# Optimization experiments

Measured on AMD Instinct MI355X. Metric: run time of the kernel, lower is better.

## Reference

```python
import jax, jax.numpy as jnp
import numpy as np

D = 64      # node_input_dim == node_hidden_dim
EIN = 16    # edge_input_dim
EH = 64     # edge_hidden_dim
NL, NR = 5000, 15000
EL, ER = 50000, 150000
STEPS = 6
EPS = 1e-5
SLOPE = 0.01


def _ln(x, g, b):
    mu = jnp.mean(x, axis=-1, keepdims=True)
    v = jnp.mean((x - mu) ** 2, axis=-1, keepdims=True)
    return (x - mu) / jnp.sqrt(v + EPS) * g + b


def _lrelu(x):
    return jnp.where(x > 0, x, SLOPE * x)


def setup_inputs() -> dict:
    key = jax.random.key(0)
    ks = jax.random.split(key, 32)

    def n(k, shape, fan_in):
        return jax.random.normal(k, shape, jnp.float32) * (fan_in ** -0.5)

    return {
        'lig_n_feat': jax.random.normal(ks[0], (NL, D), jnp.float32),
        'lig_e_feat': jax.random.normal(ks[1], (EL, EIN), jnp.float32),
        'lig_src': jax.random.randint(ks[2], (EL,), 0, NL),
        'lig_dst': jax.random.randint(ks[3], (EL,), 0, NL),
        'rec_n_feat': jax.random.normal(ks[4], (NR, D), jnp.float32),
        'rec_e_feat': jax.random.normal(ks[5], (ER, EIN), jnp.float32),
        'rec_src': jax.random.randint(ks[6], (ER,), 0, NR),
        'rec_dst': jax.random.randint(ks[7], (ER,), 0, NR),
        'mask': jax.random.uniform(ks[8], (NL, NR), jnp.float32),
        # linear0
        'W0': n(ks[9], (D, D), D), 'b0': jnp.zeros((D,), jnp.float32),
        # edge network: Linear(EIN,EH) -> ReLU -> Linear(EH, D*D)
        'We1': n(ks[10], (EH, EIN), EIN), 'be1': jnp.zeros((EH,), jnp.float32),
        'We2': n(ks[11], (D * D, EH), EH), 'be2': jnp.zeros((D * D,), jnp.float32),
        # NNConv residual fc (no bias) and conv bias
        'resW': n(ks[12], (D, D), D), 'conv_b': jnp.zeros((D,), jnp.float32),
        # message layer Linear(2D, D)
        'msgW': n(ks[13], (D, 2 * D), 2 * D), 'msgb': jnp.zeros((D,), jnp.float32),
        # attention projections (no bias)
        'Qlig': n(ks[14], (D, D), D), 'Klig': n(ks[15], (D, D), D), 'Vlig': n(ks[16], (D, D), D),
        'Qrec': n(ks[17], (D, D), D), 'Krec': n(ks[18], (D, D), D), 'Vrec': n(ks[19], (D, D), D),
        # final LayerNorms
        'g_lig': jnp.ones((D,), jnp.float32), 'b_lig': jnp.zeros((D,), jnp.float32),
        'g_rec': jnp.ones((D,), jnp.float32), 'b_rec': jnp.zeros((D,), jnp.float32),
    }


def _gather_branch(x, efeat, src, dst, n_nodes, W0, b0, We1, be1, We2, be2, resW, conv_b, msgW, msgb):
    # per-edge weight matrices from edge MLP: [E, D, D] (in x out)
    We = jax.nn.relu(efeat @ We1.T + be1) @ We2.T + be2
    We = We.reshape(-1, D, D)
    h = jax.nn.relu(x @ W0.T + b0)
    for _ in range(STEPS):
        msg = jnp.einsum('ei,eio->eo', h[src], We)          # gather + per-edge transform
        agg = jax.ops.segment_sum(msg, dst, num_segments=n_nodes)  # scatter-sum
        m = jax.nn.relu(agg + h @ resW.T + conv_b)           # NNConv residual + bias, relu
        h = jnp.concatenate([m, h], axis=1) @ msgW.T + msgb  # message_layer
    return h + x


def reference(lig_n_feat, lig_e_feat, lig_src, lig_dst, rec_n_feat, rec_e_feat, rec_src, rec_dst,
              mask, W0, b0, We1, be1, We2, be2, resW, conv_b, msgW, msgb,
              Qlig, Klig, Vlig, Qrec, Krec, Vrec, g_lig, b_lig, g_rec, b_rec):
    lig_Fv = _gather_branch(lig_n_feat, lig_e_feat, lig_src, lig_dst, NL,
                            W0, b0, We1, be1, We2, be2, resW, conv_b, msgW, msgb)
    rec_Fv = _gather_branch(rec_n_feat, rec_e_feat, rec_src, rec_dst, NR,
                            W0, b0, We1, be1, We2, be2, resW, conv_b, msgW, msgb)
    hl = _ln(lig_Fv, g_lig, b_lig)
    hr = _ln(rec_Fv, g_rec, b_rec)
    # lig attends to rec
    ql, kr, vr = _lrelu(hl @ Qlig.T), _lrelu(hr @ Krec.T), hr @ Vrec.T
    a = mask * (ql @ kr.T) - 1000.0 * (1.0 - mask)
    att_lig = jax.nn.softmax(a, axis=1) @ vr
    # rec attends to lig
    qr, kl, vl = _lrelu(hr @ Qrec.T), _lrelu(hl @ Klig.T), hl @ Vlig.T
    mt = mask.T
    a2 = mt * (qr @ kl.T) - 1000.0 * (1.0 - mt)
    att_rec = jax.nn.softmax(a2, axis=1) @ vl
    return (_ln(att_lig, g_lig, b_lig), _ln(att_rec, g_rec, b_rec))
```

## Files before the change

### kernel.cpp

```cpp
#include <hip/hip_runtime.h>
#include <hip/hip_bf16.h>

typedef unsigned short ushort_t;
typedef __attribute__((ext_vector_type(8))) short short8_t;
typedef __attribute__((ext_vector_type(4))) float f32x4;
typedef __attribute__((ext_vector_type(4))) unsigned uint4_t;

#define NLIG 5000
#define NREC 15000
#define NTOT 20000
#define ELIG 50000
#define EREC 150000
#define ETOT 200000
#define VSTRIDE 20160

__device__ __forceinline__ float us2f(ushort_t u){
  union { float f; unsigned int i; } x; x.i = ((unsigned int)u) << 16; return x.f;
}
__device__ __forceinline__ ushort_t f2us(float f){
  __hip_bfloat16 b = __float2bfloat16(f);
  return *reinterpret_cast<ushort_t*>(&b);
}
__device__ __forceinline__ unsigned pkbf(float a, float b){
  return (unsigned)f2us(a) | ((unsigned)f2us(b) << 16);
}
__device__ __forceinline__ float wsum64(float v){
#pragma unroll
  for (int s = 32; s >= 1; s >>= 1) v += __shfl_xor(v, s, 64);
  return v;
}
__device__ __forceinline__ f32x4 mfma32(short8_t a, short8_t b, f32x4 c){
  return __builtin_amdgcn_mfma_f32_16x16x32_bf16(a, b, c, 0, 0, 0);
}
__device__ __forceinline__ int geti(const int* __restrict__ p, int i, int i64){
  return i64 ? p[2*i] : p[i];
}

__global__ void kdetect2(const unsigned* __restrict__ xw, const unsigned* __restrict__ iw,
                         int* __restrict__ flagp){
  const int lane = threadIdx.x;
  unsigned w = xw[lane];
  int e0 = (int)((w >> 7) & 0xFF);
  int hit = (e0 >= 100 && e0 <= 134) ? 1 : 0;
  int zodd = ((lane & 1) && iw[lane] == 0u) ? 1 : 0;
#pragma unroll
  for (int s = 32; s >= 1; s >>= 1){
    hit  += __shfl_xor(hit,  s, 64);
    zodd += __shfl_xor(zodd, s, 64);
  }
  if (lane == 0){
    flagp[0] = (hit  >= 40) ? 1 : 0;
    flagp[1] = (zodd >= 24) ? 1 : 0;
  }
}

__global__ void ksent(float* __restrict__ out, int n, float c){
  int i = blockIdx.x*256 + threadIdx.x;
  if (i < n) out[i] = c;
}

__global__ void kcvt_x(const void* __restrict__ lx, const void* __restrict__ rx,
                       const int* __restrict__ flagp, float* __restrict__ xall){
  const int flag = flagp[0];
  const int idx = blockIdx.x*256 + threadIdx.x;
  const void* src; int local;
  if (idx < NLIG*64){ src = lx; local = idx; } else { src = rx; local = idx - NLIG*64; }
  float v;
  if (flag) v = us2f(((const ushort_t*)src)[local]);
  else      v = ((const float*)src)[local];
  xall[idx] = v;
}

struct Srcs { const void* p[20]; };
__global__ void kcvt_w(Srcs S, const int* __restrict__ flagp, float* __restrict__ wcvt){
  const int bounds[21] = {0,4096,4160,5184,5248,267392,271488,275584,275648,283840,
                          283904,288000,292096,296192,300288,304384,308480,308544,308608,308672,308736};
  const int flag = flagp[0];
  const int idx = blockIdx.x*256 + threadIdx.x;
  if (idx >= 308736) return;
  int seg = 0;
#pragma unroll
  for (int s = 1; s < 20; ++s) if (idx >= bounds[s]) seg = s;
  const void* src = S.p[0];
#pragma unroll
  for (int s = 1; s < 20; ++s) if (seg == s) src = S.p[s];
  const int local = idx - bounds[seg];
  float v;
  if (flag) v = us2f(((const ushort_t*)src)[local]);
  else      v = ((const float*)src)[local];
  wcvt[idx] = v;
}

#define W_W0    0
#define W_B0    4096
#define W_WE1   4160
#define W_BE1   5184
#define W_WE2   5248
#define W_BE2   267392
#define W_RESW  271488
#define W_CONVB 275584
#define W_MSGW  275648
#define W_MSGB  283840
#define W_QLIG  283904
#define W_KLIG  288000
#define W_VLIG  292096
#define W_QREC  296192
#define W_KREC  300288
#define W_VREC  304384
#define W_GLIG  308480
#define W_BLIG  308544
#define W_GREC  308608
#define W_BREC  308672

__global__ void kWpk(const float* __restrict__ We2f, ushort_t* __restrict__ Wpk){
  int oidx = blockIdx.x*256 + threadIdx.x;
  int j = oidx & 7, lane = (oidx >> 3) & 63, p = (oidx >> 9) & 1;
  int t = (oidx >> 10) & 3, kb = oidx >> 12;
  int o = t*16 + (lane & 15);
  int gik = kb*32 + (lane >> 4)*8 + j;
  int i = gik >> 6, k = gik & 63;
  float v = We2f[(size_t)(i*64 + o)*64 + k];
  ushort_t hi = f2us(v);
  Wpk[oidx] = p ? f2us(v - us2f(hi)) : hi;
}

__global__ void kh0(const float* __restrict__ xall, const float* __restrict__ W0f,
                    const float* __restrict__ b0f, float* __restrict__ h){
  __shared__ float xr[4][64];
  const int lane = threadIdx.x & 63, wv = threadIdx.x >> 6;
  const int n = blockIdx.x*4 + wv;
  xr[wv][lane] = xall[(size_t)n*64 + lane];
  __syncthreads();
  float acc = b0f[lane];
  const float* wr = W0f + lane*64;
#pragma unroll
  for (int i = 0; i < 64; ++i) acc += xr[wv][i] * wr[i];
  h[(size_t)n*64 + lane] = acc > 0.f ? acc : 0.f;
}

__global__ void khist(const int* __restrict__ ldst, const int* __restrict__ rdst,
                      const int* __restrict__ flagp, int* __restrict__ counts){
  const int i64 = flagp[1];
  const int e = blockIdx.x*256 + threadIdx.x;
  if (e >= ETOT) return;
  int dstg = (e < ELIG) ? geti(ldst, e, i64) : geti(rdst, e - ELIG, i64) + NLIG;
  atomicAdd(&counts[dstg], 1);
}

__global__ __launch_bounds__(1024) void kscan(const int* __restrict__ counts, int* __restrict__ offs){
  __shared__ int part[1024];
  const int tid = threadIdx.x;
  const int PER = 20;
  int loc[PER]; int s = 0;
#pragma unroll
  for (int j = 0; j < PER; ++j){ int idx = tid*PER + j; int v = (idx < NTOT) ? counts[idx] : 0; loc[j] = s; s += v; }
  part[tid] = s;
  __syncthreads();
  for (int d = 1; d < 1024; d <<= 1){
    int add = (tid >= d) ? part[tid - d] : 0;
    __syncthreads();
    part[tid] += add;
    __syncthreads();
  }
  int pre = (tid > 0) ? part[tid - 1] : 0;
#pragma unroll
  for (int j = 0; j < PER; ++j){ int idx = tid*PER + j; if (idx < NTOT) offs[idx] = pre + loc[j]; }
  if (tid == 1023) offs[NTOT] = part[1023];
}

__global__ void kfill(const int* __restrict__ lsrc, const int* __restrict__ ldst,
                      const int* __restrict__ rsrc, const int* __restrict__ rdst,
                      const void* __restrict__ lef, const void* __restrict__ ref_,
                      const int* __restrict__ offs, int* __restrict__ cursor,
                      const int* __restrict__ flagp,
                      int* __restrict__ e_srcn, float* __restrict__ ef_srt){
  const int flag = flagp[0];
  const int i64  = flagp[1];
  const int e = blockIdx.x*256 + threadIdx.x;
  if (e >= ETOT) return;
  int srcg, dstg, le; const void* efb;
  if (e < ELIG){ srcg = geti(lsrc, e, i64); dstg = geti(ldst, e, i64); efb = lef; le = e; }
  else {
    int e2 = e - ELIG;
    srcg = geti(rsrc, e2, i64) + NLIG; dstg = geti(rdst, e2, i64) + NLIG; efb = ref_; le = e2;
  }
  int pos = offs[dstg] + atomicAdd(&cursor[dstg], 1);
  e_srcn[pos] = srcg;
  float* efd = ef_srt + (size_t)pos*16;
  if (flag){
    const ushort_t* efp = (const ushort_t*)efb + (size_t)le*16;
#pragma unroll
    for (int c = 0; c < 16; ++c) efd[c] = us2f(efp[c]);
  } else {
    const float* efp = (const float*)efb + (size_t)le*16;
#pragma unroll
    for (int c = 0; c < 16; ++c) efd[c] = efp[c];
  }
}

__global__ __launch_bounds__(1024)
void kstep(const float* __restrict__ hin, float* __restrict__ hout,
           const int* __restrict__ offs, const int* __restrict__ e_srcn,
           const float* __restrict__ ef_srt,
           const ushort_t* __restrict__ Wpk,
           const float* __restrict__ We1f, const float* __restrict__ be1f,
           const float* __restrict__ resWf, const float* __restrict__ convbf,
           const float* __restrict__ msgWf, const float* __restrict__ msgbf,
           const float* __restrict__ be2f){
  __shared__ alignas(16) char sbuf[65536];
  __shared__ float h_lds[1024];
  __shared__ float Hs_lds[1024];
  __shared__ float m_lds[1024];
  __shared__ float cbf[64], mbf[64];

  const int tid = threadIdx.x, lane = tid & 63, wv = tid >> 6;
  const int n0 = blockIdx.x * 16;

  h_lds[tid] = hin[(size_t)n0*64 + tid];
  if (tid < 64){ cbf[tid] = convbf[tid]; mbf[tid] = msgbf[tid]; }

  float w1r[16];
#pragma unroll
  for (int c = 0; c < 16; ++c) w1r[c] = We1f[lane*16 + c];
  const float b1 = be1f[lane];

  float sacc[64];
#pragma unroll
  for (int i = 0; i < 64; ++i) sacc[i] = 0.f;
  float hs = 0.f;
  {
    const int v = n0 + wv;
    const int jb = offs[v], je = offs[v+1];
    for (int j = jb; j < je; ++j){
      const int sn = e_srcn[j];
      const float* efp = ef_srt + (size_t)j*16;
      float zl = b1;
#pragma unroll
      for (int c = 0; c < 16; ++c) zl += efp[c] * w1r[c];
      zl = zl > 0.f ? zl : 0.f;
      hs += hin[(size_t)sn*64 + lane];
      const float4* hp = (const float4*)(hin + (size_t)sn*64);
#pragma unroll
      for (int i4 = 0; i4 < 16; ++i4){
        float4 hv = hp[i4];
        sacc[i4*4+0] += hv.x * zl;
        sacc[i4*4+1] += hv.y * zl;
        sacc[i4*4+2] += hv.z * zl;
        sacc[i4*4+3] += hv.w * zl;
      }
    }
    Hs_lds[wv*64 + lane] = hs;
  }

  const int r15 = lane & 15, g4 = lane >> 4;
  const int tW = wv & 3, kq = wv >> 2;
  f32x4 acc; acc[0]=0.f; acc[1]=0.f; acc[2]=0.f; acc[3]=0.f;
  const unsigned sswz = ((unsigned)(wv & 7)) << 4;
  const unsigned rswz = ((unsigned)(r15 & 7)) << 4;
#pragma unroll
  for (int c = 0; c < 4; ++c){
#pragma unroll
    for (int ii = 0; ii < 16; ++ii){
      float v = sacc[c*16 + ii];
      ushort_t hi16 = f2us(v);
      unsigned off = ((unsigned)(wv*2048 + (ii*64 + lane)*2)) ^ sswz;
      *(ushort_t*)(sbuf + off) = hi16;
      *(ushort_t*)(sbuf + 32768 + off) = f2us(v - us2f(hi16));
    }
    __syncthreads();
    for (int kk = 0; kk < 8; ++kk){
      const int lk = kq*256 + kk*32;
      const int kb = c*32 + kq*8 + kk;
      const unsigned aoff = ((unsigned)(r15*2048 + (lk + g4*8)*2)) ^ rswz;
      const short8_t ah = *(const short8_t*)(sbuf + aoff);
      const short8_t al = *(const short8_t*)(sbuf + 32768 + aoff);
      const ushort_t* bp = Wpk + (size_t)(kb*4 + tW)*1024 + lane*8;
      const short8_t bh = *(const short8_t*)(bp);
      const short8_t bl = *(const short8_t*)(bp + 512);
      acc = mfma32(ah, bh, acc);
      acc = mfma32(ah, bl, acc);
      acc = mfma32(al, bh, acc);
    }
    __syncthreads();
  }

  float* redf  = (float*)sbuf;
  float* be2s  = (float*)(sbuf + 16384);
  float* resWt = (float*)(sbuf + 32768);
#pragma unroll
  for (int q = 0; q < 4; ++q)
    redf[kq*1024 + (g4*4 + q)*64 + tW*16 + r15] = acc[q];
  for (int idx = tid; idx < 4096; idx += 1024){
    be2s[idx] = be2f[idx];
    resWt[(idx & 63)*65 + (idx >> 6)] = resWf[idx];
  }
  __syncthreads();
  {
    float aggv = cbf[lane];
#pragma unroll
    for (int k4 = 0; k4 < 4; ++k4) aggv += redf[k4*1024 + wv*64 + lane];
    float t1 = 0.f, t2 = 0.f;
#pragma unroll 8
    for (int i = 0; i < 64; ++i){
      t1 += Hs_lds[wv*64 + i] * be2s[i*64 + lane];
      t2 += h_lds[wv*64 + i]  * resWt[i*65 + lane];
    }
    float mv = aggv + t1 + t2;
    m_lds[wv*64 + lane] = mv > 0.f ? mv : 0.f;
  }
  __syncthreads();
  float* msgWt = (float*)sbuf;
  for (int idx = tid; idx < 8192; idx += 1024)
    msgWt[(idx & 127)*65 + (idx >> 7)] = msgWf[idx];
  __syncthreads();
  {
    float hn = mbf[lane];
#pragma unroll 8
    for (int i = 0; i < 64; ++i){
      hn += m_lds[wv*64 + i] * msgWt[i*65 + lane];
      hn += h_lds[wv*64 + i] * msgWt[(64 + i)*65 + lane];
    }
    hout[(size_t)(n0 + wv)*64 + lane] = hn;
  }
}

__global__ void kfvproj(const float* __restrict__ h, const float* __restrict__ xall,
    const float* __restrict__ wcvt,
    ushort_t* __restrict__ qbh, ushort_t* __restrict__ qbl,
    ushort_t* __restrict__ kbh, ushort_t* __restrict__ kbl,
    ushort_t* __restrict__ vbT){
  __shared__ float hr[4][64];
  const int lane = threadIdx.x & 63, wv = threadIdx.x >> 6;
  const int n = blockIdx.x*4 + wv;
  const bool isLig = n < NLIG;
  const float fv = h[(size_t)n*64 + lane] + xall[(size_t)n*64 + lane];
  const float mu = wsum64(fv) * (1.f/64.f);
  const float dd = fv - mu;
  const float var = wsum64(dd*dd) * (1.f/64.f);
  const float gg = wcvt[(isLig ? W_GLIG : W_GREC) + lane];
  const float bb = wcvt[(isLig ? W_BLIG : W_BREC) + lane];
  const float hl = dd * rsqrtf(var + 1e-5f) * gg + bb;
  hr[wv][lane] = hl;
  __syncthreads();
  const float* Qw = wcvt + (isLig ? W_QLIG : W_QREC) + lane*64;
  const float* Kw = wcvt + (isLig ? W_KLIG : W_KREC) + lane*64;
  const float* Vw = wcvt + (isLig ? W_VLIG : W_VREC) + lane*64;
  float qa = 0.f, ka = 0.f, va = 0.f;
#pragma unroll
  for (int i = 0; i < 64; ++i){
    const float hv = hr[wv][i];
    qa += hv * Qw[i];
    ka += hv * Kw[i];
    va += hv * Vw[i];
  }
  qa = qa > 0.f ? qa : 0.01f*qa;
  ka = ka > 0.f ? ka : 0.01f*ka;
  const size_t o = (size_t)n*64 + lane;
  ushort_t qh = f2us(qa); qbh[o] = qh; qbl[o] = f2us(qa - us2f(qh));
  ushort_t kh = f2us(ka); kbh[o] = kh; kbl[o] = f2us(ka - us2f(kh));
  vbT[(size_t)lane*VSTRIDE + n] = f2us(va);
}

template<int DIRN>
__global__ __launch_bounds__(512, 2)
void kattn(const ushort_t* __restrict__ qbh, const ushort_t* __restrict__ qbl,
           const ushort_t* __restrict__ kbh, const ushort_t* __restrict__ kbl,
           const ushort_t* __restrict__ vbT, const void* __restrict__ maskp,
           const int* __restrict__ flagp,
           const float* __restrict__ gwf, const float* __restrict__ bwf,
           float* __restrict__ out){
  constexpr int R   = DIRN ? NREC : NLIG;
  constexpr int C   = DIRN ? NLIG : NREC;
  constexpr int RNB = DIRN ? NLIG : 0;
  constexpr int CNB = DIRN ? 0 : NLIG;
  __shared__ float mred[8][16], lred[8][16];
  __shared__ float ored[8][64][17];

  const int flag = flagp[0];
  const int tid = threadIdx.x, lane = tid & 63, wv = tid >> 6;
  const int r15 = lane & 15, g4 = lane >> 4;
  const int rbase = blockIdx.x * 16;
  int rn = rbase + r15; if (rn > R-1) rn = R-1;

  const ushort_t* qph = qbh + (size_t)(RNB + rn)*64;
  const ushort_t* qpl = qbl + (size_t)(RNB + rn)*64;
  const short8_t qh0a = *(const short8_t*)(qph + g4*8);
  const short8_t qh0b = *(const short8_t*)(qph + 32 + g4*8);
  const short8_t ql0a = *(const short8_t*)(qpl + g4*8);
  const short8_t ql0b = *(const short8_t*)(qpl + 32 + g4*8);

  const int srcA = (((g4 & 1) * 2)     << 4) + r15;
  const int srcB = (((g4 & 1) * 2 + 1) << 4) + r15;
  const bool hiBank = (g4 >> 1) != 0;

  float mrun = -1e30f, lrun = 0.f;
  f32x4 oacc[4];
#pragma unroll
  for (int t = 0; t < 4; ++t){ oacc[t][0]=0.f; oacc[t][1]=0.f; oacc[t][2]=0.f; oacc[t][3]=0.f; }

  for (int cb = wv*32; cb < C; cb += 256){
    int cn0 = cb + r15;      if (cn0 > C-1) cn0 = C-1;
    int cn1 = cb + 16 + r15; if (cn1 > C-1) cn1 = C-1;
    const ushort_t* kp0h = kbh + (size_t)(CNB + cn0)*64;
    const ushort_t* kp0l = kbl + (size_t)(CNB + cn0)*64;
    const ushort_t* kp1h = kbh + (size_t)(CNB + cn1)*64;
    const ushort_t* kp1l = kbl + (size_t)(CNB + cn1)*64;
    f32x4 st0; st0[0]=0.f; st0[1]=0.f; st0[2]=0.f; st0[3]=0.f;
    f32x4 st1 = st0;
    {
      short8_t ka_ = *(const short8_t*)(kp0h + g4*8);
      short8_t kb_ = *(const short8_t*)(kp0h + 32 + g4*8);
      st0 = mfma32(ka_, qh0a, st0); st0 = mfma32(kb_, qh0b, st0);
      st0 = mfma32(ka_, ql0a, st0); st0 = mfma32(kb_, ql0b, st0);
      short8_t kc_ = *(const short8_t*)(kp0l + g4*8);
      short8_t kd_ = *(const short8_t*)(kp0l + 32 + g4*8);
      st0 = mfma32(kc_, qh0a, st0); st0 = mfma32(kd_, qh0b, st0);
    }
    {
      short8_t ka_ = *(const short8_t*)(kp1h + g4*8);
      short8_t kb_ = *(const short8_t*)(kp1h + 32 + g4*8);
      st1 = mfma32(ka_, qh0a, st1); st1 = mfma32(kb_, qh0b, st1);
      st1 = mfma32(ka_, ql0a, st1); st1 = mfma32(kb_, ql0b, st1);
      short8_t kc_ = *(const short8_t*)(kp1l + g4*8);
      short8_t kd_ = *(const short8_t*)(kp1l + 32 + g4*8);
      st1 = mfma32(kc_, qh0a, st1); st1 = mfma32(kd_, qh0b, st1);
    }
    float sv0[4], sv1[4]; float tmax = -1e30f;
#pragma unroll
    for (int j = 0; j < 4; ++j){
      const int c0 = cb + g4*4 + j, c1 = cb + 16 + g4*4 + j;
      const int c0c = c0 > C-1 ? C-1 : c0, c1c = c1 > C-1 ? C-1 : c1;
      size_t m0, m1;
      if (DIRN == 0){ m0 = (size_t)rn*NREC + c0c; m1 = (size_t)rn*NREC + c1c; }
      else          { m0 = (size_t)c0c*NREC + rn; m1 = (size_t)c1c*NREC + rn; }
      float mv0, mv1;
      if (flag){ mv0 = us2f(((const ushort_t*)maskp)[m0]); mv1 = us2f(((const ushort_t*)maskp)[m1]); }
      else     { mv0 = ((const float*)maskp)[m0];          mv1 = ((const float*)maskp)[m1]; }
      sv0[j] = (c0 < C) ? mv0 * (st0[j] + 1000.f) : -1e30f;
      sv1[j] = (c1 < C) ? mv1 * (st1[j] + 1000.f) : -1e30f;
      tmax = fmaxf(tmax, fmaxf(sv0[j], sv1[j]));
    }
    tmax = fmaxf(tmax, __shfl_xor(tmax, 16, 64));
    tmax = fmaxf(tmax, __shfl_xor(tmax, 32, 64));
    const float mnew = fmaxf(mrun, tmax);
    const float corr = __expf(mrun - mnew);
    float ps0[4], ps1[4], psum = 0.f;
#pragma unroll
    for (int j = 0; j < 4; ++j){
      ps0[j] = __expf(sv0[j] - mnew); psum += ps0[j];
      ps1[j] = __expf(sv1[j] - mnew); psum += ps1[j];
    }
    psum += __shfl_xor(psum, 16, 64);
    psum += __shfl_xor(psum, 32, 64);
    lrun = lrun * corr + psum;
    mrun = mnew;
    const unsigned pk0 = pkbf(ps0[0], ps0[1]);
    const unsigned pk1 = pkbf(ps0[2], ps0[3]);
    const unsigned pk2 = pkbf(ps1[0], ps1[1]);
    const unsigned pk3 = pkbf(ps1[2], ps1[3]);
    const unsigned a0 = (unsigned)__shfl((int)pk0, srcA, 64);
    const unsigned a2 = (unsigned)__shfl((int)pk2, srcA, 64);
    const unsigned a1 = (unsigned)__shfl((int)pk1, srcA, 64);
    const unsigned a3 = (unsigned)__shfl((int)pk3, srcA, 64);
    const unsigned b0 = (unsigned)__shfl((int)pk0, srcB, 64);
    const unsigned b2 = (unsigned)__shfl((int)pk2, srcB, 64);
    const unsigned b1 = (unsigned)__shfl((int)pk1, srcB, 64);
    const unsigned b3 = (unsigned)__shfl((int)pk3, srcB, 64);
    uint4_t pw;
    pw[0] = hiBank ? a2 : a0;
    pw[1] = hiBank ? a3 : a1;
    pw[2] = hiBank ? b2 : b0;
    pw[3] = hiBank ? b3 : b1;
    const short8_t pf8 = *reinterpret_cast<const short8_t*>(&pw);
    const ushort_t* vtb = vbT + (size_t)(CNB + cb + g4*8);
#pragma unroll
    for (int t = 0; t < 4; ++t){
#pragma unroll
      for (int q = 0; q < 4; ++q) oacc[t][q] *= corr;
      const short8_t af = *(const short8_t*)(vtb + (size_t)(t*16 + r15)*VSTRIDE);
      oacc[t] = mfma32(af, pf8, oacc[t]);
    }
  }

  if (g4 == 0){ mred[wv][r15] = mrun; lred[wv][r15] = lrun; }
#pragma unroll
  for (int t = 0; t < 4; ++t)
#pragma unroll
    for (int q = 0; q < 4; ++q)
      ored[wv][t*16 + g4*4 + q][r15] = oacc[t][q];
  __syncthreads();

  for (int rr = 2*wv; rr <= 2*wv + 1; ++rr){
    float mstar = -1e30f;
#pragma unroll
    for (int w = 0; w < 8; ++w) mstar = fmaxf(mstar, mred[w][rr]);
    float lstar = 0.f, ov = 0.f;
#pragma unroll
    for (int w = 0; w < 8; ++w){
      const float e = __expf(mred[w][rr] - mstar);
      lstar += lred[w][rr] * e;
      ov    += ored[w][lane][rr] * e;
    }
    const float att = ov / lstar;
    const float mu = wsum64(att) * (1.f/64.f);
    const float dd = att - mu;
    const float var = wsum64(dd*dd) * (1.f/64.f);
    const float y = dd * rsqrtf(var + 1e-5f) * gwf[lane] + bwf[lane];
    const int rg = rbase + rr;
    if (rg < R) out[(size_t)rg*64 + lane] = y;
  }
}

extern "C" void kernel_launch(void* const* d_in, const int* in_sizes, int n_in,
                              void* d_out, int out_size, void* d_ws, size_t ws_size,
                              hipStream_t stream){
  const int expsz[29] = {320000,800000,50000,50000,960000,2400000,150000,150000,75000000,
                         4096,64,1024,64,262144,4096,4096,64,8192,64,
                         4096,4096,4096,4096,4096,4096,64,64,64,64};
  bool ok = (n_in == 29);
  if (ok) for (int i = 0; i < 29; ++i) if (in_sizes[i] != expsz[i]) ok = false;
  if (!ok){
    ksent<<<(out_size + 255)/256, 256, 0, stream>>>((float*)d_out, out_size, 10.0f);
    return;
  }

  const void* lig_n = d_in[0];
  const void* lig_e = d_in[1];
  const int* lig_src = (const int*)d_in[2];
  const int* lig_dst = (const int*)d_in[3];
  const void* rec_n = d_in[4];
  const void* rec_e = d_in[5];
  const int* rec_src = (const int*)d_in[6];
  const int* rec_dst = (const int*)d_in[7];
  const void* mask = d_in[8];

  char* p = (char*)d_ws;
  auto carve = [&](size_t bytes)->char*{ char* r = p; p += (bytes + 255) & ~(size_t)255; return r; };
  float*    xall  = (float*)   carve((size_t)NTOT*64*4);
  float*    wcvt  = (float*)   carve((size_t)308736*4);
  float*    h_a   = (float*)   carve((size_t)NTOT*64*4);
  float*    h_b   = (float*)   carve((size_t)NTOT*64*4);
  ushort_t* Wpk   = (ushort_t*)carve((size_t)524288*2);
  ushort_t* qbh   = (ushort_t*)carve((size_t)NTOT*64*2);
  ushort_t* qbl   = (ushort_t*)carve((size_t)NTOT*64*2);
  ushort_t* kbh   = (ushort_t*)carve((size_t)NTOT*64*2);
  ushort_t* kbl   = (ushort_t*)carve((size_t)NTOT*64*2);
  ushort_t* vbT   = (ushort_t*)carve((size_t)64*VSTRIDE*2);
  int*      flag  = (int*)     carve(256);
  int*      counts= (int*)     carve((size_t)2*NTOT*4);
  int*      cursor= counts + NTOT;
  int*      offs  = (int*)     carve((size_t)(NTOT+1)*4);
  int*      e_srcn= (int*)     carve((size_t)ETOT*4);
  float*    ef_srt= (float*)   carve((size_t)ETOT*16*4);

  if ((size_t)(p - (char*)d_ws) > ws_size){
    ksent<<<(out_size + 255)/256, 256, 0, stream>>>((float*)d_out, out_size, 20.0f);
    return;
  }

  Srcs S;
  for (int i = 0; i < 20; ++i) S.p[i] = d_in[9 + i];

  hipMemsetAsync(counts, 0, (size_t)2*NTOT*4, stream);
  hipMemsetAsync(vbT, 0, (size_t)64*VSTRIDE*2, stream);
  kdetect2<<<1, 64, 0, stream>>>((const unsigned*)lig_n, (const unsigned*)lig_src, flag);
  kcvt_x<<<NTOT*64/256, 256, 0, stream>>>(lig_n, rec_n, flag, xall);
  kcvt_w<<<(308736 + 255)/256, 256, 0, stream>>>(S, flag, wcvt);
  kWpk<<<2048, 256, 0, stream>>>(wcvt + W_WE2, Wpk);
  kh0<<<NTOT/4, 256, 0, stream>>>(xall, wcvt + W_W0, wcvt + W_B0, h_a);
  khist<<<(ETOT + 255)/256, 256, 0, stream>>>(lig_dst, rec_dst, flag, counts);
  kscan<<<1, 1024, 0, stream>>>(counts, offs);
  kfill<<<(ETOT + 255)/256, 256, 0, stream>>>(lig_src, lig_dst, rec_src, rec_dst,
                                              lig_e, rec_e, offs, cursor, flag, e_srcn, ef_srt);
  float* hi = h_a; float* ho = h_b;
  for (int s = 0; s < 6; ++s){
    kstep<<<NTOT/16, 1024, 0, stream>>>(hi, ho, offs, e_srcn, ef_srt, Wpk,
                                        wcvt + W_WE1, wcvt + W_BE1, wcvt + W_RESW,
                                        wcvt + W_CONVB, wcvt + W_MSGW, wcvt + W_MSGB,
                                        wcvt + W_BE2);
    float* t = hi; hi = ho; ho = t;
  }
  kfvproj<<<NTOT/4, 256, 0, stream>>>(hi, xall, wcvt, qbh, qbl, kbh, kbl, vbT);
  kattn<0><<<(NLIG + 15)/16, 512, 0, stream>>>(qbh, qbl, kbh, kbl, vbT, mask, flag,
                                               wcvt + W_GLIG, wcvt + W_BLIG,
                                               (float*)d_out);
  kattn<1><<<(NREC + 15)/16, 512, 0, stream>>>(qbh, qbl, kbh, kbl, vbT, mask, flag,
                                               wcvt + W_GREC, wcvt + W_BREC,
                                               (float*)d_out + (size_t)NLIG*64);
}
```

Baseline: 2.451 ms.

## Stage mask tiles in shared memory with coalesced vector loads per column block

Each 256-column block of the attention mask is now loaded cooperatively by the whole workgroup into a shared-memory tile using float4 loads, then read from LDS in the softmax step. Before, each lane did scattered scalar global loads, and in the transposed direction these were strided. The aim is coalesced mask traffic. In exchange it adds two block-wide barriers per column tile, plus about 16 KB more LDS, and drops the occupancy hint from launch_bounds.

```diff
diff --git a/kernel.cpp b/kernel.cpp
--- a/kernel.cpp
+++ b/kernel.cpp
@@ -362,7 +362,7 @@
 }
 
 template<int DIRN>
-__global__ __launch_bounds__(512, 2)
+__global__ __launch_bounds__(512)
 void kattn(const ushort_t* __restrict__ qbh, const ushort_t* __restrict__ qbl,
            const ushort_t* __restrict__ kbh, const ushort_t* __restrict__ kbl,
            const ushort_t* __restrict__ vbT, const void* __restrict__ maskp,
@@ -375,6 +375,7 @@
   constexpr int CNB = DIRN ? 0 : NLIG;
   __shared__ float mred[8][16], lred[8][16];
   __shared__ float ored[8][64][17];
+  __shared__ float m_tile[16][257];
 
   const int flag = flagp[0];
   const int tid = threadIdx.x, lane = tid & 63, wv = tid >> 6;
@@ -398,7 +399,51 @@
 #pragma unroll
   for (int t = 0; t < 4; ++t){ oacc[t][0]=0.f; oacc[t][1]=0.f; oacc[t][2]=0.f; oacc[t][3]=0.f; }
 
-  for (int cb = wv*32; cb < C; cb += 256){
+  for (int tb = 0; tb < C; tb += 256){
+    __syncthreads();
+    if (DIRN == 0){
+      const int row = tid >> 5;
+      int r = rbase + row; if (r > R-1) r = R-1;
+      int col = tb + (tid & 31)*8; if (col > C-8) col = C-8;
+      const size_t base = (size_t)r*NREC + col;
+      const int cl0 = col - tb;
+      if (flag){
+        const ushort_t* mp = (const ushort_t*)maskp + base;
+#pragma unroll
+        for (int j = 0; j < 8; ++j) m_tile[row][cl0 + j] = us2f(mp[j]);
+      } else {
+        const float* mp = (const float*)maskp + base;
+        const float4 v0 = *(const float4*)mp;
+        const float4 v1 = *(const float4*)(mp + 4);
+        m_tile[row][cl0+0]=v0.x; m_tile[row][cl0+1]=v0.y;
+        m_tile[row][cl0+2]=v0.z; m_tile[row][cl0+3]=v0.w;
+        m_tile[row][cl0+4]=v1.x; m_tile[row][cl0+5]=v1.y;
+        m_tile[row][cl0+6]=v1.z; m_tile[row][cl0+7]=v1.w;
+      }
+    } else {
+      const int cl = tid >> 1, half = tid & 1;
+      int c = tb + cl; if (c > C-1) c = C-1;
+      int r0 = rbase + half*8; if (r0 > R-8) r0 = R-8;
+      const size_t base = (size_t)c*NREC + r0;
+      const int rr0 = r0 - rbase;
+      const int cc = c - tb;
+      if (flag){
+        const ushort_t* mp = (const ushort_t*)maskp + base;
+#pragma unroll
+        for (int j = 0; j < 8; ++j) m_tile[rr0 + j][cc] = us2f(mp[j]);
+      } else {
+        const float* mp = (const float*)maskp + base;
+        const float4 v0 = *(const float4*)mp;
+        const float4 v1 = *(const float4*)(mp + 4);
+        m_tile[rr0+0][cc]=v0.x; m_tile[rr0+1][cc]=v0.y;
+        m_tile[rr0+2][cc]=v0.z; m_tile[rr0+3][cc]=v0.w;
+        m_tile[rr0+4][cc]=v1.x; m_tile[rr0+5][cc]=v1.y;
+        m_tile[rr0+6][cc]=v1.z; m_tile[rr0+7][cc]=v1.w;
+      }
+    }
+    __syncthreads();
+
+    const int cb = tb + wv*32;
     int cn0 = cb + r15;      if (cn0 > C-1) cn0 = C-1;
     int cn1 = cb + 16 + r15; if (cn1 > C-1) cn1 = C-1;
     const ushort_t* kp0h = kbh + (size_t)(CNB + cn0)*64;
@@ -429,13 +474,8 @@
 #pragma unroll
     for (int j = 0; j < 4; ++j){
       const int c0 = cb + g4*4 + j, c1 = cb + 16 + g4*4 + j;
-      const int c0c = c0 > C-1 ? C-1 : c0, c1c = c1 > C-1 ? C-1 : c1;
-      size_t m0, m1;
-      if (DIRN == 0){ m0 = (size_t)rn*NREC + c0c; m1 = (size_t)rn*NREC + c1c; }
-      else          { m0 = (size_t)c0c*NREC + rn; m1 = (size_t)c1c*NREC + rn; }
-      float mv0, mv1;
-      if (flag){ mv0 = us2f(((const ushort_t*)maskp)[m0]); mv1 = us2f(((const ushort_t*)maskp)[m1]); }
-      else     { mv0 = ((const float*)maskp)[m0];          mv1 = ((const float*)maskp)[m1]; }
+      const float mv0 = m_tile[r15][wv*32 + g4*4 + j];
+      const float mv1 = m_tile[r15][wv*32 + 16 + g4*4 + j];
       sv0[j] = (c0 < C) ? mv0 * (st0[j] + 1000.f) : -1e30f;
       sv1[j] = (c1 < C) ? mv1 * (st1[j] + 1000.f) : -1e30f;
       tmax = fmaxf(tmax, fmaxf(sv0[j], sv1[j]));
```

Result: faster. 2.283 ms (-6.9%).
